# Optimization experiments

Hardware: AMD Instinct MI355X
Metric: run time of the kernel (lower is better)

Reference implementation:

```python
import jax, jax.numpy as jnp
import numpy as np

B, SQ, SK = 2, 2048, 2048
DQ = DK = DV = DM = DOUT = 1024
H = 16
DHEAD = DM // H


def setup_inputs() -> dict:
    key = jax.random.key(0)
    ks = jax.random.split(key, 12)
    s = 0.02
    return {
        "Q": jax.random.normal(ks[0], (B, SQ, DQ), jnp.float32),
        "K": jax.random.normal(ks[1], (B, SK, DK), jnp.float32),
        "V": jax.random.normal(ks[2], (B, SK, DV), jnp.float32),
        "mask": jax.random.randint(ks[3], (B, 1, SK), 0, 2, jnp.int32),
        "Wq": jax.random.normal(ks[4], (DQ, DM), jnp.float32) * s,
        "bq": jnp.zeros((DM,), jnp.float32),
        "Wk": jax.random.normal(ks[5], (DK, DM), jnp.float32) * s,
        "bk": jnp.zeros((DM,), jnp.float32),
        "Wv": jax.random.normal(ks[6], (DV, DM), jnp.float32) * s,
        "bv": jnp.zeros((DM,), jnp.float32),
        "Wo": jax.random.normal(ks[7], (DM, DOUT), jnp.float32) * s,
        "bo": jnp.zeros((DOUT,), jnp.float32),
    }


def reference(Q, K, V, mask, Wq, bq, Wk, bk, Wv, bv, Wo, bo):
    b, sq, _ = Q.shape
    # QKV projections then split heads: (B, S, D) -> (B, H, S, d_k)
    q = (Q @ Wq + bq).reshape(b, sq, H, DHEAD).transpose(0, 2, 1, 3)
    k = (K @ Wk + bk).reshape(b, -1, H, DHEAD).transpose(0, 2, 1, 3)
    v = (V @ Wv + bv).reshape(b, -1, H, DHEAD).transpose(0, 2, 1, 3)
    # scores: (B, H, Sq, Sk)
    scores = jnp.einsum("bhqd,bhkd->bhqk", q, k) / np.sqrt(DHEAD).astype(np.float32)
    m = mask[:, None]  # (B,1,1,Sk), broadcast over heads and queries
    scores = jnp.where(m == 0, -jnp.inf, scores)
    attn = jax.nn.softmax(scores, axis=-1)
    out = jnp.einsum("bhqk,bhkd->bhqd", attn, v)
    out = out.transpose(0, 2, 1, 3).reshape(b, sq, DM)
    return out @ Wo + bo
```

## Files before the change

kernel.cpp:

```cpp
#include <hip/hip_runtime.h>
#include <hip/hip_bf16.h>

#define SQn 2048
#define SKn 2048
#define DMn 1024
#define NHn 16
#define DHn 64

typedef __attribute__((ext_vector_type(8))) short bf16x8;
typedef __attribute__((ext_vector_type(4))) float f32x4;

#define QSCALE 0.1803368801f

#define FBAR()                                     \
  __builtin_amdgcn_sched_barrier(0);               \
  asm volatile("s_barrier" ::: "memory");          \
  __builtin_amdgcn_sched_barrier(0)

__device__ __forceinline__ short f2bf(float f) {
  union { float f; unsigned u; } a; a.f = f;
  return (short)((a.u + 0x7FFFu + ((a.u >> 16) & 1u)) >> 16);
}

__device__ __forceinline__ unsigned cvt_pk_bf16(float lo, float hi) {
  unsigned r;
  asm("v_cvt_pk_bf16_f32 %0, %1, %2" : "=v"(r) : "v"(lo), "v"(hi));
  return r;
}

__device__ __forceinline__ void gload16(const void* g, void* l) {
  __builtin_amdgcn_global_load_lds(
      (__attribute__((address_space(1))) void*)g,
      (__attribute__((address_space(3))) void*)l, 16, 0, 0);
}

#define NCASTB 12288
__global__ __launch_bounds__(256) void prep(
    const float* __restrict__ Q, const float* __restrict__ K, const float* __restrict__ V,
    const float* __restrict__ W0, const float* __restrict__ W1,
    const float* __restrict__ W2, const float* __restrict__ W3,
    const int* __restrict__ mask,
    short* __restrict__ qkvOut, short* __restrict__ WtBase,
    int* __restrict__ inv, int* __restrict__ Lb) {
  const int blk = blockIdx.x;
  const int tid = threadIdx.x;
  __shared__ float t[32][33];
  __shared__ int part[256];
  __shared__ int base[256];
  __shared__ int totL;

  if (blk < NCASTB) {
    const int n4each = (2 * 2048 * 1024) / 4;
    int i = blk * 256 + tid;
    const float* src;
    int j = i;
    if (i < n4each) src = Q;
    else if (i < 2 * n4each) { src = K; j = i - n4each; }
    else { src = V; j = i - 2 * n4each; }
    float4 f = ((const float4*)src)[j];
    short4 o;
    o.x = f2bf(f.x); o.y = f2bf(f.y); o.z = f2bf(f.z); o.w = f2bf(f.w);
    ((short4*)qkvOut)[i] = o;
  } else if (blk < NCASTB + 4096) {
    const int tt = blk - NCASTB;
    const int z = tt >> 10;
    const int rem = tt & 1023;
    const float* W = (z == 0) ? W0 : (z == 1) ? W1 : (z == 2) ? W2 : W3;
    short* Wt = WtBase + (size_t)z * DMn * DMn;
    const int bx = (rem & 31) * 32;
    const int by = (rem >> 5) * 32;
    const int tx = tid & 31, ty = tid >> 5;
#pragma unroll
    for (int j = 0; j < 4; ++j)
      t[ty + j * 8][tx] = W[(size_t)(by + ty + j * 8) * DMn + bx + tx];
    __syncthreads();
#pragma unroll
    for (int j = 0; j < 4; ++j)
      Wt[(size_t)(bx + ty + j * 8) * DMn + by + tx] = f2bf(t[tx][ty + j * 8]);
  } else {
    const int b = blk - NCASTB - 4096;
    const int* m = mask + b * SKn;
    int v[8];
    int s0 = 0;
#pragma unroll
    for (int j = 0; j < 8; ++j) { v[j] = m[tid * 8 + j] ? 1 : 0; s0 += v[j]; }
    part[tid] = s0;
    __syncthreads();
    if (tid == 0) {
      int acc = 0;
      for (int i = 0; i < 256; ++i) { base[i] = acc; acc += part[i]; }
      Lb[b] = acc;
      totL = acc;
    }
    __syncthreads();
    int acc = base[tid];
    int* ip = inv + b * SKn;
#pragma unroll
    for (int j = 0; j < 8; ++j) {
      int s = tid * 8 + j;
      int c = v[j] ? acc : (totL + s - acc);
      ip[c] = s;
      acc += v[j];
    }
  }
}

__global__ __launch_bounds__(512) void gemm_bt3(
    const short* __restrict__ A0, const short* __restrict__ A1, const short* __restrict__ A2,
    const short* __restrict__ B0, const short* __restrict__ B1, const short* __restrict__ B2,
    const float* __restrict__ c0, const float* __restrict__ c1, const float* __restrict__ c2,
    short* __restrict__ O0, short* __restrict__ O1, short* __restrict__ O2,
    const int* __restrict__ invp, const int* __restrict__ Lp) {
  constexpr int K = 1024;
  const int z = blockIdx.z;
  const int bm = blockIdx.x * 128, bn = blockIdx.y * 128;

  if (z != 0 && (bm & 2047) >= Lp[bm >> 11]) return;

  const short* A  = (z == 0) ? A0 : (z == 1) ? A1 : A2;
  const short* Bt = (z == 0) ? B0 : (z == 1) ? B1 : B2;
  const float* bias = (z == 0) ? c0 : (z == 1) ? c1 : c2;
  short* Cout = (z == 0) ? O0 : (z == 1) ? O1 : O2;

  __shared__ short As[128 * 32];
  __shared__ short Bs[128 * 32];
  const int tid = threadIdx.x;
  const int lane = tid & 63;
  const int wid = tid >> 6;
  const int wr = wid >> 2, wc = wid & 3;

  f32x4 acc[4][2] = {};

  const int srow = tid >> 2;
  const int scol = (tid & 3) * 8;
  int srcRow = bm + srow;
  if (z != 0) srcRow = (srcRow & ~2047) | invp[srcRow];
  const short* Arow = A + (size_t)srcRow * K;
  const short* Brow = Bt + (size_t)(bn + srow) * K;

  for (int k0 = 0; k0 < K; k0 += 32) {
    __syncthreads();
    gload16(Arow + k0 + scol, As + tid * 8);
    gload16(Brow + k0 + scol, Bs + tid * 8);
    __syncthreads();

    bf16x8 a[4], b[2];
    const int rowA = wr * 64 + (lane & 15);
    const int rowB = wc * 32 + (lane & 15);
    const int ko = (lane >> 4) * 8;
#pragma unroll
    for (int m = 0; m < 4; ++m) a[m] = *(const bf16x8*)(As + (rowA + m * 16) * 32 + ko);
#pragma unroll
    for (int n = 0; n < 2; ++n) b[n] = *(const bf16x8*)(Bs + (rowB + n * 16) * 32 + ko);
#pragma unroll
    for (int m = 0; m < 4; ++m)
#pragma unroll
      for (int n = 0; n < 2; ++n)
        acc[m][n] = __builtin_amdgcn_mfma_f32_16x16x32_bf16(a[m], b[n], acc[m][n], 0, 0, 0);
  }

  const int crow0 = bm + wr * 64 + ((lane >> 4) * 4);
  const int ccol0 = bn + wc * 32 + (lane & 15);
  float bv[2];
#pragma unroll
  for (int n = 0; n < 2; ++n) bv[n] = bias[ccol0 + n * 16];
#pragma unroll
  for (int m = 0; m < 4; ++m)
#pragma unroll
    for (int i = 0; i < 4; ++i) {
      int row = crow0 + m * 16 + i;
      int bb = row >> 11, s = row & 2047;
#pragma unroll
      for (int n = 0; n < 2; ++n) {
        int col = ccol0 + n * 16;
        float val = acc[m][n][i] + bv[n];
        int hh = col >> 6, d = col & 63;
        if (z == 2) {
          Cout[((((size_t)bb * NHn + hh) * DHn + d) << 11) + s] = f2bf(val);
        } else {
          if (z == 0) val *= QSCALE;
          Cout[((((size_t)bb * NHn + hh) * SQn + s) << 6) + d] = f2bf(val);
        }
      }
    }
}

__global__ __launch_bounds__(256) void gemm_n64(const short* __restrict__ A,
                                                const short* __restrict__ Bt,
                                                const float* __restrict__ bias,
                                                float* __restrict__ C) {
  constexpr int K = 1024, N = 1024;
  __shared__ short As[2][128 * 32];
  __shared__ short Bs[2][64 * 32];
  const int tid = threadIdx.x;
  const int lane = tid & 63;
  const int wid = tid >> 6;
  const int wr = wid >> 1, wc = wid & 1;
  const int bm = blockIdx.x * 128, bn = blockIdx.y * 64;

  f32x4 acc[4][2] = {};

  const int srow = tid >> 2;
  const int scol = (tid & 3) * 8;
  const short* Ag = A + (size_t)bm * K;
  const short* Bg = Bt + (size_t)bn * K;

#define GSTG(buf, k0)                                                             \
  gload16(Ag + (size_t)srow * K + (k0) + scol,        As[buf] + tid * 8);         \
  gload16(Ag + (size_t)(srow + 64) * K + (k0) + scol, As[buf] + 2048 + tid * 8);  \
  gload16(Bg + (size_t)srow * K + (k0) + scol,        Bs[buf] + tid * 8);

  GSTG(0, 0);
  GSTG(1, 32);

  const int rowA = wr * 64 + (lane & 15);
  const int rowB = wc * 32 + (lane & 15);
  const int ko = (lane >> 4) * 8;

  for (int t = 0; t < 32; ++t) {
    const int cur = t & 1;
    if (t < 31) asm volatile("s_waitcnt vmcnt(3)" ::: "memory");
    else        asm volatile("s_waitcnt vmcnt(0)" ::: "memory");
    FBAR();

    bf16x8 a[4], b[2];
#pragma unroll
    for (int m = 0; m < 4; ++m) a[m] = *(const bf16x8*)(As[cur] + (rowA + m * 16) * 32 + ko);
#pragma unroll
    for (int n = 0; n < 2; ++n) b[n] = *(const bf16x8*)(Bs[cur] + (rowB + n * 16) * 32 + ko);
    __builtin_amdgcn_s_setprio(1);
#pragma unroll
    for (int m = 0; m < 4; ++m)
#pragma unroll
      for (int n = 0; n < 2; ++n)
        acc[m][n] = __builtin_amdgcn_mfma_f32_16x16x32_bf16(a[m], b[n], acc[m][n], 0, 0, 0);
    __builtin_amdgcn_s_setprio(0);

    FBAR();
    if (t < 30) { GSTG(cur, t * 32 + 64); }
  }
#undef GSTG

  const int crow0 = bm + wr * 64 + ((lane >> 4) * 4);
  const int ccol0 = bn + wc * 32 + (lane & 15);
#pragma unroll
  for (int m = 0; m < 4; ++m)
#pragma unroll
    for (int n = 0; n < 2; ++n) {
      int col = ccol0 + n * 16;
      float bv = bias[col];
#pragma unroll
      for (int i = 0; i < 4; ++i) {
        int row = crow0 + m * 16 + i;
        C[(size_t)row * N + col] = acc[m][n][i] + bv;
      }
    }
}

__global__ __launch_bounds__(512) void attn(const short* __restrict__ q,
                                            const short* __restrict__ k,
                                            const short* __restrict__ vt,
                                            const int* __restrict__ Lb,
                                            short* __restrict__ out) {
  __shared__ short Ks[2][64 * 64];
  __shared__ short Vs[2][64 * 64];
  __shared__ short Ps[8][16 * 64];

  const int tid = threadIdx.x;
  const int lane = tid & 63;
  const int w = tid >> 6;
  const int l = (blockIdx.x & 7) * 64 + (blockIdx.x >> 3);
  const int bh = l >> 4;
  const int qt = l & 15;
  const int h = bh & 15;
  const int b = bh >> 4;
  const size_t hoff = (size_t)bh * (SQn * DHn);

  const int c_ = lane & 15, g_ = lane >> 4;
  const int swz = (c_ & 7) << 4;

  const int L = Lb[b];
  const int nt = (L + 63) >> 6;
  const int lastt = nt - 1;

  bf16x8 qf[2];
  {
    const short* qp = q + hoff + (size_t)(qt * 128 + w * 16 + c_) * DHn + g_ * 8;
    qf[0] = *(const bf16x8*)qp;
    qf[1] = *(const bf16x8*)(qp + 32);
  }

  const int r0 = tid >> 3;
  const int gch = (tid & 7) ^ (r0 & 7);
  const size_t kO = (size_t)r0 * DHn + gch * 8;
  const size_t vO = (size_t)r0 * SKn + gch * 8;
  const int ldsO = tid * 8;

  float mrun = -1e30f;
  float lrun = 0.f;
  f32x4 o[4] = {};
  char* PwB = (char*)Ps[w];

#define STAGE(buf, kbase, vbase)            \
  gload16((kbase) + kO, &Ks[buf][ldsO]);    \
  gload16((vbase) + vO, &Vs[buf][ldsO]);

  const short* kpre = k + hoff;
  const short* vpre = vt + hoff;
  STAGE(0, kpre, vpre);
  kpre += 64 * DHn;
  vpre += 64;
  __syncthreads();

  int cur = 0;
  for (int kt = 0; kt < nt; ++kt) {
    if (kt + 1 < nt) {
      STAGE(cur ^ 1, kpre, vpre);
      kpre += 64 * DHn;
      vpre += 64;
    }

    const short* Kc = Ks[cur];
    const short* Vc = Vs[cur];

    f32x4 s[4];
    __builtin_amdgcn_s_setprio(1);
#pragma unroll
    for (int n = 0; n < 4; ++n) {
      f32x4 a = {};
      int key = n * 16 + c_;
#pragma unroll
      for (int kc = 0; kc < 2; ++kc) {
        int slot = (kc * 4 + g_) ^ (key & 7);
        bf16x8 kf = *(const bf16x8*)(Kc + key * 64 + slot * 8);
        a = __builtin_amdgcn_mfma_f32_16x16x32_bf16(kf, qf[kc], a, 0, 0, 0);
      }
      s[n] = a;
    }
    __builtin_amdgcn_s_setprio(0);

    if (kt == lastt) {
      const int kb = kt * 64 + g_ * 4;
#pragma unroll
      for (int n = 0; n < 4; ++n) {
        const int k0i = kb + n * 16;
        s[n][0] = (k0i + 0 < L) ? s[n][0] : -1e30f;
        s[n][1] = (k0i + 1 < L) ? s[n][1] : -1e30f;
        s[n][2] = (k0i + 2 < L) ? s[n][2] : -1e30f;
        s[n][3] = (k0i + 3 < L) ? s[n][3] : -1e30f;
      }
    }

    float pmax = fmaxf(fmaxf(s[0][0], s[0][1]), fmaxf(s[0][2], s[0][3]));
#pragma unroll
    for (int n = 1; n < 4; ++n)
      pmax = fmaxf(pmax, fmaxf(fmaxf(s[n][0], s[n][1]), fmaxf(s[n][2], s[n][3])));

    if (!__all(pmax - mrun <= 8.f)) {
      float pm = fmaxf(pmax, __shfl_xor(pmax, 16));
      pm = fmaxf(pm, __shfl_xor(pm, 32));
      float mn = fmaxf(mrun, pm);
      float sc = __builtin_amdgcn_exp2f(mrun - mn);
      mrun = mn;
      lrun *= sc;
      float scB[4];
#pragma unroll
      for (int i = 0; i < 4; ++i) scB[i] = __shfl(sc, g_ * 4 + i);
#pragma unroll
      for (int n = 0; n < 4; ++n)
#pragma unroll
        for (int i = 0; i < 4; ++i) o[n][i] *= scB[i];
    }

    float lsum = 0.f;
#pragma unroll
    for (int n = 0; n < 4; ++n) {
      float p0 = __builtin_amdgcn_exp2f(s[n][0] - mrun);
      float p1 = __builtin_amdgcn_exp2f(s[n][1] - mrun);
      float p2 = __builtin_amdgcn_exp2f(s[n][2] - mrun);
      float p3 = __builtin_amdgcn_exp2f(s[n][3] - mrun);
      lsum += (p0 + p1) + (p2 + p3);
      uint2 pk;
      pk.x = cvt_pk_bf16(p0, p1);
      pk.y = cvt_pk_bf16(p2, p3);
      *(uint2*)(PwB + ((c_ * 128) | ((n * 32 + g_ * 8) ^ swz))) = pk;
    }
    lrun += lsum;

    __builtin_amdgcn_s_setprio(1);
#pragma unroll
    for (int ks = 0; ks < 2; ++ks) {
      bf16x8 pf = *(const bf16x8*)(PwB + ((c_ * 128) | ((ks * 64 + g_ * 16) ^ swz)));
#pragma unroll
      for (int n = 0; n < 4; ++n) {
        int d = n * 16 + c_;
        int slot = (ks * 4 + g_) ^ (d & 7);
        bf16x8 vf = *(const bf16x8*)(Vc + d * 64 + slot * 8);
        o[n] = __builtin_amdgcn_mfma_f32_16x16x32_bf16(pf, vf, o[n], 0, 0, 0);
      }
    }
    __builtin_amdgcn_s_setprio(0);

    __syncthreads();
    cur ^= 1;
  }

  lrun += __shfl_xor(lrun, 16);
  lrun += __shfl_xor(lrun, 32);
  float lB[4];
#pragma unroll
  for (int i = 0; i < 4; ++i) lB[i] = __shfl(lrun, g_ * 4 + i);
#pragma unroll
  for (int n = 0; n < 4; ++n) {
#pragma unroll
    for (int i = 0; i < 4; ++i) {
      int srow = qt * 128 + w * 16 + g_ * 4 + i;
      int d = n * 16 + c_;
      out[((size_t)b * SQn + srow) * DMn + h * 64 + d] = f2bf(o[n][i] / lB[i]);
    }
  }
#undef STAGE
}

extern "C" void kernel_launch(void* const* d_in, const int* in_sizes, int n_in,
                              void* d_out, int out_size, void* d_ws, size_t ws_size,
                              hipStream_t stream) {
  const float* Q  = (const float*)d_in[0];
  const float* K  = (const float*)d_in[1];
  const float* V  = (const float*)d_in[2];
  const int* mask = (const int*)d_in[3];
  const float* Wq = (const float*)d_in[4];
  const float* bq = (const float*)d_in[5];
  const float* Wk = (const float*)d_in[6];
  const float* bk = (const float*)d_in[7];
  const float* Wv = (const float*)d_in[8];
  const float* bv = (const float*)d_in[9];
  const float* Wo = (const float*)d_in[10];
  const float* bo = (const float*)d_in[11];

  char* ws = (char*)d_ws;
  const size_t MB = 1024 * 1024;
  short* Qb  = (short*)(ws + 0 * MB);
  short* Wqt = (short*)(ws + 24 * MB);
  short* Wkt = (short*)(ws + 26 * MB);
  short* Wvt = (short*)(ws + 28 * MB);
  short* Wot = (short*)(ws + 30 * MB);
  short* qp  = (short*)(ws + 32 * MB);
  short* kp  = (short*)(ws + 40 * MB);
  short* vpt = (short*)(ws + 48 * MB);
  int*   invp = (int*)(ws + 56 * MB);
  int*   Lbp  = (int*)(ws + 56 * MB + 16384);
  short* Kb  = Qb + 4 * MB;
  short* Vb  = Qb + 8 * MB;
  short* ao  = Qb;

  prep<<<NCASTB + 4096 + 2, 256, 0, stream>>>(Q, K, V, Wq, Wk, Wv, Wo, mask,
                                              Qb, Wqt, invp, Lbp);

  gemm_bt3<<<dim3(32, 8, 3), 512, 0, stream>>>(Qb, Kb, Vb, Wqt, Wkt, Wvt,
                                               bq, bk, bv, qp, kp, vpt,
                                               invp, Lbp);

  attn<<<512, 512, 0, stream>>>(qp, kp, vpt, Lbp, ao);

  gemm_n64<<<dim3(32, 16), 256, 0, stream>>>(ao, Wot, bo, (float*)d_out);
}
```

Baseline: 108.4 us.

## Widen QKV GEMM tile to 128x256 and double-buffer LDS loads

After: 136.9 us. +26.3%, slower.

```diff
diff --git a/kernel.cpp b/kernel.cpp
--- a/kernel.cpp
+++ b/kernel.cpp
@@ -113,7 +113,7 @@
     const int* __restrict__ invp, const int* __restrict__ Lp) {
   constexpr int K = 1024;
   const int z = blockIdx.z;
-  const int bm = blockIdx.x * 128, bn = blockIdx.y * 128;
+  const int bm = blockIdx.x * 128, bn = blockIdx.y * 256;
 
   if (z != 0 && (bm & 2047) >= Lp[bm >> 11]) return;
 
@@ -122,48 +122,64 @@
   const float* bias = (z == 0) ? c0 : (z == 1) ? c1 : c2;
   short* Cout = (z == 0) ? O0 : (z == 1) ? O1 : O2;
 
-  __shared__ short As[128 * 32];
-  __shared__ short Bs[128 * 32];
+  __shared__ short As[2][128 * 32];
+  __shared__ short Bs[2][256 * 32];
   const int tid = threadIdx.x;
   const int lane = tid & 63;
   const int wid = tid >> 6;
   const int wr = wid >> 2, wc = wid & 3;
 
-  f32x4 acc[4][2] = {};
+  f32x4 acc[4][4] = {};
 
   const int srow = tid >> 2;
   const int scol = (tid & 3) * 8;
   int srcRow = bm + srow;
   if (z != 0) srcRow = (srcRow & ~2047) | invp[srcRow];
   const short* Arow = A + (size_t)srcRow * K;
-  const short* Brow = Bt + (size_t)(bn + srow) * K;
-
-  for (int k0 = 0; k0 < K; k0 += 32) {
-    __syncthreads();
-    gload16(Arow + k0 + scol, As + tid * 8);
-    gload16(Brow + k0 + scol, Bs + tid * 8);
-    __syncthreads();
-
-    bf16x8 a[4], b[2];
-    const int rowA = wr * 64 + (lane & 15);
-    const int rowB = wc * 32 + (lane & 15);
-    const int ko = (lane >> 4) * 8;
-#pragma unroll
-    for (int m = 0; m < 4; ++m) a[m] = *(const bf16x8*)(As + (rowA + m * 16) * 32 + ko);
-#pragma unroll
-    for (int n = 0; n < 2; ++n) b[n] = *(const bf16x8*)(Bs + (rowB + n * 16) * 32 + ko);
+  const short* Brow0 = Bt + (size_t)(bn + srow) * K;
+  const short* Brow1 = Brow0 + (size_t)128 * K;
+
+#define GSTG(buf, k0)                                      \
+  gload16(Arow + (k0) + scol,  As[buf] + tid * 8);         \
+  gload16(Brow0 + (k0) + scol, Bs[buf] + tid * 8);         \
+  gload16(Brow1 + (k0) + scol, Bs[buf] + 4096 + tid * 8);
+
+  GSTG(0, 0);
+  GSTG(1, 32);
+
+  const int rowA = wr * 64 + (lane & 15);
+  const int rowB = wc * 64 + (lane & 15);
+  const int ko = (lane >> 4) * 8;
+
+  for (int t = 0; t < 32; ++t) {
+    const int cur = t & 1;
+    if (t < 31) asm volatile("s_waitcnt vmcnt(3)" ::: "memory");
+    else        asm volatile("s_waitcnt vmcnt(0)" ::: "memory");
+    FBAR();
+
+    bf16x8 a[4], b[4];
+#pragma unroll
+    for (int m = 0; m < 4; ++m) a[m] = *(const bf16x8*)(As[cur] + (rowA + m * 16) * 32 + ko);
+#pragma unroll
+    for (int n = 0; n < 4; ++n) b[n] = *(const bf16x8*)(Bs[cur] + (rowB + n * 16) * 32 + ko);
+    __builtin_amdgcn_s_setprio(1);
 #pragma unroll
     for (int m = 0; m < 4; ++m)
 #pragma unroll
-      for (int n = 0; n < 2; ++n)
+      for (int n = 0; n < 4; ++n)
         acc[m][n] = __builtin_amdgcn_mfma_f32_16x16x32_bf16(a[m], b[n], acc[m][n], 0, 0, 0);
-  }
+    __builtin_amdgcn_s_setprio(0);
+
+    FBAR();
+    if (t < 30) { GSTG(cur, t * 32 + 64); }
+  }
+#undef GSTG
 
   const int crow0 = bm + wr * 64 + ((lane >> 4) * 4);
-  const int ccol0 = bn + wc * 32 + (lane & 15);
-  float bv[2];
-#pragma unroll
-  for (int n = 0; n < 2; ++n) bv[n] = bias[ccol0 + n * 16];
+  const int ccol0 = bn + wc * 64 + (lane & 15);
+  float bv[4];
+#pragma unroll
+  for (int n = 0; n < 4; ++n) bv[n] = bias[ccol0 + n * 16];
 #pragma unroll
   for (int m = 0; m < 4; ++m)
 #pragma unroll
@@ -171,7 +187,7 @@
       int row = crow0 + m * 16 + i;
       int bb = row >> 11, s = row & 2047;
 #pragma unroll
-      for (int n = 0; n < 2; ++n) {
+      for (int n = 0; n < 4; ++n) {
         int col = ccol0 + n * 16;
         float val = acc[m][n][i] + bv[n];
         int hh = col >> 6, d = col & 63;
@@ -457,7 +473,7 @@
   prep<<<NCASTB + 4096 + 2, 256, 0, stream>>>(Q, K, V, Wq, Wk, Wv, Wo, mask,
                                               Qb, Wqt, invp, Lbp);
 
-  gemm_bt3<<<dim3(32, 8, 3), 512, 0, stream>>>(Qb, Kb, Vb, Wqt, Wkt, Wvt,
+  gemm_bt3<<<dim3(32, 4, 3), 512, 0, stream>>>(Qb, Kb, Vb, Wqt, Wkt, Wvt,
                                                bq, bk, bv, qp, kp, vpt,
                                                invp, Lbp);
 
```
